# Optimization experiments

Measured on AMD Instinct MI355X. Metric: run time of the kernel, lower is better.

The kernel has to match this reference:

```python
import jax, jax.numpy as jnp
from jax import lax
import numpy as np

DN = ('NDHWC', 'DHWIO', 'NDHWC')

def conv3d(x, w, b, stride=1):
    return lax.conv_general_dilated(x, w, (stride,) * 3, 'SAME', dimension_numbers=DN) + b

def convT3d(x, w, b, stride=2):
    return lax.conv_transpose(x, w, (stride,) * 3, 'SAME', dimension_numbers=DN) + b

def prelu(x, a):
    return jnp.where(x > 0, x, a * x)

def bn(x, g, be, m, v):
    # keras BatchNormalization, inference mode, epsilon=1e-3
    return (x - m) * g * lax.rsqrt(v + 1e-3) + be

def res_unit(x, c1w, c1b, c2w, c2b, g, be, m, v, a):
    # VQVAEResidualUnit: relu(x + PReLU(BN(conv2(swish(conv1(x))))))
    h = jax.nn.swish(conv3d(x, c1w, c1b))
    h = prelu(bn(conv3d(h, c2w, c2b), g, be, m, v), a)
    return jax.nn.relu(x + h)

def _forward(x, ec0_w, ec0_b, er0_c1w, er0_c1b, er0_c2w, er0_c2b, er0_g, er0_be, er0_m, er0_v, er0_a, ec1_w, ec1_b, er1_c1w, er1_c1b, er1_c2w, er1_c2b, er1_g, er1_be, er1_m, er1_v, er1_a, eo_w, eo_b, eo_a, codebook, dc0_w, dc0_b, dc0_a, dr0_c1w, dr0_c1b, dr0_c2w, dr0_c2b, dr0_g, dr0_be, dr0_m, dr0_v, dr0_a, du0_w, du0_b, dr1_c1w, dr1_c1b, dr1_c2w, dr1_c2b, dr1_g, dr1_be, dr1_m, dr1_v, dr1_a, du1_w, du1_b):
    # ----- Encoder -----
    h = jax.nn.relu(conv3d(x, ec0_w, ec0_b, stride=2))   # [B,64,64,64,64]
    h = res_unit(h, er0_c1w, er0_c1b, er0_c2w, er0_c2b, er0_g, er0_be, er0_m, er0_v, er0_a)
    h = jax.nn.relu(conv3d(h, ec1_w, ec1_b, stride=2))   # [B,32,32,32,128]
    h = res_unit(h, er1_c1w, er1_c1b, er1_c2w, er1_c2b, er1_g, er1_be, er1_m, er1_v, er1_a)
    z = prelu(conv3d(h, eo_w, eo_b), eo_a)               # [B,32,32,32,64] latent
    # ----- NSVQ (inference: hard codebook lookup) -----
    D = z.shape[-1]
    flat = z.reshape(-1, D)                              # [N, 64], N = B*32^3
    dist = (flat * flat).sum(1, keepdims=True) + (codebook * codebook).sum(1) - 2.0 * (flat @ codebook.T)  # [N, K]
    idx = jnp.argmin(dist, axis=1)
    zq = codebook[idx].reshape(z.shape)
    K = codebook.shape[0]
    p = jnp.zeros((K,), jnp.float32).at[idx].add(1.0) / flat.shape[0]
    perplexity = jnp.exp(-jnp.sum(p * jnp.log(p + 1e-12)))
    # ----- Decoder -----
    h = prelu(conv3d(zq, dc0_w, dc0_b), dc0_a)           # [B,32,32,32,128]
    h = res_unit(h, dr0_c1w, dr0_c1b, dr0_c2w, dr0_c2b, dr0_g, dr0_be, dr0_m, dr0_v, dr0_a)
    h = jax.nn.relu(convT3d(h, du0_w, du0_b))            # [B,64,64,64,64]
    h = res_unit(h, dr1_c1w, dr1_c1b, dr1_c2w, dr1_c2b, dr1_g, dr1_be, dr1_m, dr1_v, dr1_a)
    recon = convT3d(h, du1_w, du1_b)                     # [B,128,128,128,1]
    return recon, perplexity

def setup_inputs() -> dict:
    key = jax.random.key(0)
    ks = iter(jax.random.split(key, 40))
    nrm = lambda *s: jax.random.normal(next(ks), s, jnp.float32) * 0.05
    def ru(pfx, c):
        return {pfx + '_c1w': nrm(3, 3, 3, c, c), pfx + '_c1b': jnp.zeros((c,), jnp.float32),
                pfx + '_c2w': nrm(3, 3, 3, c, c), pfx + '_c2b': jnp.zeros((c,), jnp.float32),
                pfx + '_g': jnp.ones((c,), jnp.float32), pfx + '_be': jnp.zeros((c,), jnp.float32),
                pfx + '_m': jnp.zeros((c,), jnp.float32), pfx + '_v': jnp.ones((c,), jnp.float32),
                pfx + '_a': jnp.full((c,), 0.25, jnp.float32)}
    C0, C1, D, K = 64, 128, 64, 512
    inp = {'x': jax.random.normal(next(ks), (2, 128, 128, 128, 1), jnp.float32)}
    inp.update(ec0_w=nrm(4, 4, 4, 1, C0), ec0_b=jnp.zeros((C0,), jnp.float32))
    inp.update(ru('er0', C0))
    inp.update(ec1_w=nrm(4, 4, 4, C0, C1), ec1_b=jnp.zeros((C1,), jnp.float32))
    inp.update(ru('er1', C1))
    inp.update(eo_w=nrm(3, 3, 3, C1, D), eo_b=jnp.zeros((D,), jnp.float32), eo_a=jnp.full((D,), 0.25, jnp.float32))
    inp.update(codebook=jax.random.uniform(next(ks), (K, D), jnp.float32, -1.0, 1.0) * np.sqrt(6.0 / D).astype(np.float32))
    inp.update(dc0_w=nrm(3, 3, 3, D, C1), dc0_b=jnp.zeros((C1,), jnp.float32), dc0_a=jnp.full((C1,), 0.25, jnp.float32))
    inp.update(ru('dr0', C1))
    inp.update(du0_w=nrm(4, 4, 4, C1, C0), du0_b=jnp.zeros((C0,), jnp.float32))
    inp.update(ru('dr1', C0))
    inp.update(du1_w=nrm(4, 4, 4, C0, 1), du1_b=jnp.zeros((1,), jnp.float32))
    return inp

def reference(x, ec0_w, ec0_b, er0_c1w, er0_c1b, er0_c2w, er0_c2b, er0_g, er0_be, er0_m, er0_v, er0_a, ec1_w, ec1_b, er1_c1w, er1_c1b, er1_c2w, er1_c2b, er1_g, er1_be, er1_m, er1_v, er1_a, eo_w, eo_b, eo_a, codebook, dc0_w, dc0_b, dc0_a, dr0_c1w, dr0_c1b, dr0_c2w, dr0_c2b, dr0_g, dr0_be, dr0_m, dr0_v, dr0_a, du0_w, du0_b, dr1_c1w, dr1_c1b, dr1_c2w, dr1_c2b, dr1_g, dr1_be, dr1_m, dr1_v, dr1_a, du1_w, du1_b):
    return _forward(x, ec0_w, ec0_b, er0_c1w, er0_c1b, er0_c2w, er0_c2b, er0_g, er0_be, er0_m, er0_v, er0_a, ec1_w, ec1_b, er1_c1w, er1_c1b, er1_c2w, er1_c2b, er1_g, er1_be, er1_m, er1_v, er1_a, eo_w, eo_b, eo_a, codebook, dc0_w, dc0_b, dc0_a, dr0_c1w, dr0_c1b, dr0_c2w, dr0_c2b, dr0_g, dr0_be, dr0_m, dr0_v, dr0_a, du0_w, du0_b, dr1_c1w, dr1_c1b, dr1_c2w, dr1_c2b, dr1_g, dr1_be, dr1_m, dr1_v, dr1_a, du1_w, du1_b)
```

## Files before the change

kernel.cpp:

```cpp
#include <hip/hip_runtime.h>
#include <cstdint>


typedef unsigned short bf16_t;
typedef __attribute__((ext_vector_type(8)))  short s8b;
typedef __attribute__((ext_vector_type(16))) float f32x16;

__device__ __forceinline__ float b2f(bf16_t u) { return __uint_as_float((unsigned)u << 16); }
__device__ __forceinline__ bf16_t f2b(float f) {
    unsigned x = __float_as_uint(f);
    return (bf16_t)((x + 0x7FFFu + ((x >> 16) & 1u)) >> 16);
}

__device__ __forceinline__ void split3s(float v, unsigned short& h,
                                        unsigned short& m, unsigned short& l)
{
    const unsigned uv = __float_as_uint(v);
    const float fh = __uint_as_float(uv & 0xFFFF0000u);
    const float r1 = v - fh;
    const unsigned u1 = __float_as_uint(r1);
    const float fm = __uint_as_float(u1 & 0xFFFF0000u);
    const float r2 = r1 - fm;
    h = (unsigned short)(uv >> 16);
    m = (unsigned short)(u1 >> 16);
    l = (unsigned short)(__float_as_uint(r2) >> 16);
}

__device__ __forceinline__ int wdst(int tap, int ci_, int co_, int ci, int co)
{
    const int ks = ci_ >> 4, half = (ci_ >> 3) & 1, j = ci_ & 7;
    return (((tap * (ci >> 4) + ks) * 2 + half) * co + co_) * 8 + j;
}

__global__ __launch_bounds__(256)
void wprep3(const float* __restrict__ w, bf16_t* __restrict__ h,
            bf16_t* __restrict__ m, bf16_t* __restrict__ l,
            int ci, int co, int n)
{
    const int i = blockIdx.x * 256 + threadIdx.x;
    if (i >= n) return;
    const int co_ = i % co;
    const int ci_ = (i / co) % ci;
    const int tap = i / (co * ci);
    const int dst = wdst(tap, ci_, co_, ci, co);
    unsigned short hh, mm, ll2;
    split3s(w[i], hh, mm, ll2);
    h[dst] = hh; m[dst] = mm; l[dst] = ll2;
}

__global__ __launch_bounds__(256)
void wprep_split(const float* __restrict__ w, bf16_t* __restrict__ hi,
                 bf16_t* __restrict__ lo, int ci, int co, int n)
{
    const int i = blockIdx.x * 256 + threadIdx.x;
    if (i >= n) return;
    const int co_ = i % co;
    const int ci_ = (i / co) % ci;
    const int tap = i / (co * ci);
    const float v = w[i];
    const int dst = wdst(tap, ci_, co_, ci, co);
    const bf16_t h = f2b(v);
    hi[dst] = h;
    lo[dst] = f2b(v - b2f(h));
}

template<int CIN, int COUT, int SD, int NW, int EPI>
__global__ __launch_bounds__((SD / 32) * NW * 64)
void conv3e(const float* __restrict__ xf,
            const bf16_t* __restrict__ wh, const bf16_t* __restrict__ wm,
            const bf16_t* __restrict__ wl,
            const float* __restrict__ bias,
            const float* __restrict__ g, const float* __restrict__ be,
            const float* __restrict__ mn, const float* __restrict__ vr,
            const float* __restrict__ al,
            const float* skf, float* __restrict__ of)
{
    constexpr int NT = (SD / 32) * NW * 64;
    constexpr int LP = (SD * CIN) / (4 * NT);
    constexpr int KS = CIN / 16;
    __shared__ bf16_t lh[SD * CIN], lm[SD * CIN], ll[SD * CIN];

    const int tid  = threadIdx.x;
    const int lane = tid & 63;
    const int wid  = tid >> 6;
    const int wn   = wid % NW, wm2 = wid / NW;
    const int half = lane >> 5, ln = lane & 31;
    const int w    = wm2 * 32 + ln;
    const int nwg  = gridDim.x;
    const int bid  = (blockIdx.x & 7) * (nwg >> 3) + (blockIdx.x >> 3);
    const int h    = bid % SD;
    const int d    = (bid / SD) % SD;
    const int b    = bid / (SD * SD);
    const int cout0 = wn * 64 + ln;

    int pz[9], py[9], pt[9], np = 0;
    for (int kd = 0; kd < 3; ++kd) {
        const int iz = d + kd - 1;
        if ((unsigned)iz >= (unsigned)SD) continue;
        for (int kh = 0; kh < 3; ++kh) {
            const int iy = h + kh - 1;
            if ((unsigned)iy >= (unsigned)SD) continue;
            pz[np] = iz; py[np] = iy; pt[np] = (kd * 3 + kh) * 3; ++np;
        }
    }

    f32x16 accA[2], accB[2];
#pragma unroll
    for (int i = 0; i < 16; ++i) {
        accA[0][i] = 0.f; accA[1][i] = 0.f;
        accB[0][i] = 0.f; accB[1][i] = 0.f;
    }

    float4 rg[LP];
    auto loadrow = [&](int iz, int iy) {
        const float* src = xf + ((size_t)((b * SD + iz) * SD + iy)) * SD * CIN;
#pragma unroll
        for (int j = 0; j < LP; ++j)
            rg[j] = *reinterpret_cast<const float4*>(src + (size_t)(tid + j * NT) * 4);
    };
    auto writerow = [&]() {
#pragma unroll
        for (int j = 0; j < LP; ++j) {
            const int idx = (tid + j * NT) * 4;
            const int vox = idx / CIN, ch = idx % CIN;
            ushort4 h4, m4, l4;
            split3s(rg[j].x, h4.x, m4.x, l4.x);
            split3s(rg[j].y, h4.y, m4.y, l4.y);
            split3s(rg[j].z, h4.z, m4.z, l4.z);
            split3s(rg[j].w, h4.w, m4.w, l4.w);
            const int bo = ((vox * CIN + ch) * 2) ^ ((vox & 7) << 4);
            *reinterpret_cast<ushort4*>((char*)&lh[0] + bo) = h4;
            *reinterpret_cast<ushort4*>((char*)&lm[0] + bo) = m4;
            *reinterpret_cast<ushort4*>((char*)&ll[0] + bo) = l4;
        }
    };

    loadrow(pz[0], py[0]);
    writerow();
    __syncthreads();
#pragma unroll 1
    for (int i = 0; i < np; ++i) {
        if (i + 1 < np) loadrow(pz[i + 1], py[i + 1]);
#pragma unroll
        for (int kw = 0; kw < 3; ++kw) {
            const int tap = pt[i] + kw;
            const int iw = w + kw - 1;
            const bool edge = (unsigned)iw >= (unsigned)SD;
            const int wcl = edge ? w : iw;
            const s8b zz = {};
#pragma unroll
            for (int ks = 0; ks < KS; ++ks) {
                const int bo = ((wcl * CIN + half * 8 + ks * 16) * 2) ^ ((wcl & 7) << 4);
                s8b ah  = *reinterpret_cast<const s8b*>((const char*)&lh[0] + bo);
                s8b am  = *reinterpret_cast<const s8b*>((const char*)&lm[0] + bo);
                s8b al3 = *reinterpret_cast<const s8b*>((const char*)&ll[0] + bo);
                if (edge) { ah = zz; am = zz; al3 = zz; }
                const size_t wb0 = ((size_t)((tap * KS + ks) * 2 + half) * COUT + cout0) * 8;
#pragma unroll
                for (int n2 = 0; n2 < 2; ++n2) {
                    const size_t wb = wb0 + n2 * 256;
                    const s8b bh = *reinterpret_cast<const s8b*>(wh + wb);
                    const s8b bm = *reinterpret_cast<const s8b*>(wm + wb);
                    const s8b bl = *reinterpret_cast<const s8b*>(wl + wb);
                    accA[n2] = __builtin_amdgcn_mfma_f32_32x32x16_bf16(ah, bh, accA[n2], 0, 0, 0);
                    accB[n2] = __builtin_amdgcn_mfma_f32_32x32x16_bf16(ah, bm, accB[n2], 0, 0, 0);
                    accA[n2] = __builtin_amdgcn_mfma_f32_32x32x16_bf16(am, bh, accA[n2], 0, 0, 0);
                    accB[n2] = __builtin_amdgcn_mfma_f32_32x32x16_bf16(am, bm, accB[n2], 0, 0, 0);
                    accA[n2] = __builtin_amdgcn_mfma_f32_32x32x16_bf16(al3, bh, accA[n2], 0, 0, 0);
                    accB[n2] = __builtin_amdgcn_mfma_f32_32x32x16_bf16(ah, bl, accB[n2], 0, 0, 0);
                }
            }
        }
        if (i + 1 < np) {
            __syncthreads();
            writerow();
            __syncthreads();
        }
    }

    const size_t outrow = ((size_t)((b * SD + d) * SD + h)) * SD;
#pragma unroll
    for (int n2 = 0; n2 < 2; ++n2) {
        const int cout = wn * 64 + n2 * 32 + ln;
        const float bv = bias[cout];
        float sc = 0.f, mm = 0.f, bb2 = 0.f, aa = 0.f;
        if constexpr (EPI == 3) {
            sc = g[cout] * (1.0f / sqrtf(vr[cout] + 1e-3f));
            mm = mn[cout]; bb2 = be[cout]; aa = al[cout];
        }
        if constexpr (EPI == 2) aa = al[cout];
#pragma unroll
        for (int r = 0; r < 16; ++r) {
            const int rl = (r & 3) + 8 * (r >> 2) + 4 * half;
            const size_t oe = (outrow + wm2 * 32 + rl) * COUT + cout;
            float y = accA[n2][r] + accB[n2][r] + bv;
            if constexpr (EPI == 0) y = fmaxf(y, 0.f);
            else if constexpr (EPI == 1) y = y / (1.f + expf(-y));
            else if constexpr (EPI == 2) y = y > 0.f ? y : aa * y;
            else {
                float t2 = (y - mm) * sc + bb2;
                t2 = t2 > 0.f ? t2 : aa * t2;
                y = fmaxf(skf[oe] + t2, 0.f);
            }
            of[oe] = y;
        }
    }
}

__global__ __launch_bounds__(128)
void convs2e(const float* __restrict__ xf,
             const bf16_t* __restrict__ wh, const bf16_t* __restrict__ wm,
             const bf16_t* __restrict__ wl,
             const float* __restrict__ bias, float* __restrict__ of)
{
    constexpr int NT = 128, LP = (64 * 64) / (4 * NT);
    __shared__ bf16_t lh[64 * 64], lm[64 * 64], ll[64 * 64];

    const int tid  = threadIdx.x;
    const int lane = tid & 63;
    const int wn   = tid >> 6;
    const int half = lane >> 5, ln = lane & 31;
    const int nwg  = gridDim.x;
    const int bid  = (blockIdx.x & 7) * (nwg >> 3) + (blockIdx.x >> 3);
    const int h    = bid % 32;
    const int d    = (bid / 32) % 32;
    const int b    = bid / 1024;
    const int cout0 = wn * 64 + ln;

    int pz[16], py[16], pt[16], np = 0;
    for (int kd = 0; kd < 4; ++kd) {
        const int iz = 2 * d + kd - 1;
        if ((unsigned)iz >= 64u) continue;
        for (int kh = 0; kh < 4; ++kh) {
            const int iy = 2 * h + kh - 1;
            if ((unsigned)iy >= 64u) continue;
            pz[np] = iz; py[np] = iy; pt[np] = (kd * 4 + kh) * 4; ++np;
        }
    }

    f32x16 accA[2], accB[2];
#pragma unroll
    for (int i = 0; i < 16; ++i) {
        accA[0][i] = 0.f; accA[1][i] = 0.f;
        accB[0][i] = 0.f; accB[1][i] = 0.f;
    }

    float4 rg[LP];
    auto loadrow = [&](int iz, int iy) {
        const float* src = xf + ((size_t)((b * 64 + iz) * 64 + iy)) * 64 * 64;
#pragma unroll
        for (int j = 0; j < LP; ++j)
            rg[j] = *reinterpret_cast<const float4*>(src + (size_t)(tid + j * NT) * 4);
    };
    auto writerow = [&]() {
#pragma unroll
        for (int j = 0; j < LP; ++j) {
            const int idx = (tid + j * NT) * 4;
            const int vox = idx / 64, ch = idx % 64;
            ushort4 h4, m4, l4;
            split3s(rg[j].x, h4.x, m4.x, l4.x);
            split3s(rg[j].y, h4.y, m4.y, l4.y);
            split3s(rg[j].z, h4.z, m4.z, l4.z);
            split3s(rg[j].w, h4.w, m4.w, l4.w);
            const int bo = ((vox * 64 + ch) * 2) ^ ((vox & 7) << 4);
            *reinterpret_cast<ushort4*>((char*)&lh[0] + bo) = h4;
            *reinterpret_cast<ushort4*>((char*)&lm[0] + bo) = m4;
            *reinterpret_cast<ushort4*>((char*)&ll[0] + bo) = l4;
        }
    };

    loadrow(pz[0], py[0]);
    writerow();
    __syncthreads();
#pragma unroll 1
    for (int i = 0; i < np; ++i) {
        if (i + 1 < np) loadrow(pz[i + 1], py[i + 1]);
#pragma unroll
        for (int kw = 0; kw < 4; ++kw) {
            const int tap = pt[i] + kw;
            const int iw = 2 * ln + kw - 1;
            const bool edge = (unsigned)iw >= 64u;
            const int wcl = edge ? 2 * ln : iw;
            const s8b zz = {};
#pragma unroll
            for (int ks = 0; ks < 4; ++ks) {
                const int bo = ((wcl * 64 + half * 8 + ks * 16) * 2) ^ ((wcl & 7) << 4);
                s8b ah  = *reinterpret_cast<const s8b*>((const char*)&lh[0] + bo);
                s8b am  = *reinterpret_cast<const s8b*>((const char*)&lm[0] + bo);
                s8b al3 = *reinterpret_cast<const s8b*>((const char*)&ll[0] + bo);
                if (edge) { ah = zz; am = zz; al3 = zz; }
                const size_t wb0 = ((size_t)((tap * 4 + ks) * 2 + half) * 128 + cout0) * 8;
#pragma unroll
                for (int n2 = 0; n2 < 2; ++n2) {
                    const size_t wb = wb0 + n2 * 256;
                    const s8b bh = *reinterpret_cast<const s8b*>(wh + wb);
                    const s8b bm = *reinterpret_cast<const s8b*>(wm + wb);
                    const s8b bl = *reinterpret_cast<const s8b*>(wl + wb);
                    accA[n2] = __builtin_amdgcn_mfma_f32_32x32x16_bf16(ah, bh, accA[n2], 0, 0, 0);
                    accB[n2] = __builtin_amdgcn_mfma_f32_32x32x16_bf16(ah, bm, accB[n2], 0, 0, 0);
                    accA[n2] = __builtin_amdgcn_mfma_f32_32x32x16_bf16(am, bh, accA[n2], 0, 0, 0);
                    accB[n2] = __builtin_amdgcn_mfma_f32_32x32x16_bf16(am, bm, accB[n2], 0, 0, 0);
                    accA[n2] = __builtin_amdgcn_mfma_f32_32x32x16_bf16(al3, bh, accA[n2], 0, 0, 0);
                    accB[n2] = __builtin_amdgcn_mfma_f32_32x32x16_bf16(ah, bl, accB[n2], 0, 0, 0);
                }
            }
        }
        if (i + 1 < np) {
            __syncthreads();
            writerow();
            __syncthreads();
        }
    }

    const size_t outrow = ((size_t)((b * 32 + d) * 32 + h)) * 32;
#pragma unroll
    for (int n2 = 0; n2 < 2; ++n2) {
        const int cout = wn * 64 + n2 * 32 + ln;
        const float bv = bias[cout];
#pragma unroll
        for (int r = 0; r < 16; ++r) {
            const int rl = (r & 3) + 8 * (r >> 2) + 4 * half;
            const size_t oe = (outrow + rl) * 128 + cout;
            of[oe] = fmaxf(accA[n2][r] + accB[n2][r] + bv, 0.f);
        }
    }
}

template<int CIN, int COUT, int SD, int NW, int EPI>
__global__ __launch_bounds__((SD / 32) * NW * 64)
void conv3d(const bf16_t* __restrict__ xh, const bf16_t* __restrict__ xl,
            const bf16_t* __restrict__ wh, const bf16_t* __restrict__ wl,
            const float* __restrict__ bias,
            const float* __restrict__ g, const float* __restrict__ be,
            const float* __restrict__ mn, const float* __restrict__ vr,
            const float* __restrict__ al,
            const bf16_t* skh, const bf16_t* skl,
            bf16_t* oh, bf16_t* ol)
{
    constexpr int NT = (SD / 32) * NW * 64;
    constexpr int LP = (SD * CIN) / (4 * NT);
    constexpr int KS = CIN / 16;
    __shared__ bf16_t lh[SD * CIN], ll[SD * CIN];

    const int tid  = threadIdx.x;
    const int lane = tid & 63;
    const int wid  = tid >> 6;
    const int wn   = wid % NW, wm2 = wid / NW;
    const int half = lane >> 5, ln = lane & 31;
    const int w    = wm2 * 32 + ln;
    const int nwg  = gridDim.x;
    const int bid  = (blockIdx.x & 7) * (nwg >> 3) + (blockIdx.x >> 3);
    const int h    = bid % SD;
    const int d    = (bid / SD) % SD;
    const int b    = bid / (SD * SD);
    const int cout0 = wn * 64 + ln;

    int pz[9], py[9], pt[9], np = 0;
    for (int kd = 0; kd < 3; ++kd) {
        const int iz = d + kd - 1;
        if ((unsigned)iz >= (unsigned)SD) continue;
        for (int kh = 0; kh < 3; ++kh) {
            const int iy = h + kh - 1;
            if ((unsigned)iy >= (unsigned)SD) continue;
            pz[np] = iz; py[np] = iy; pt[np] = (kd * 3 + kh) * 3; ++np;
        }
    }

    f32x16 accA[2], accB[2];
#pragma unroll
    for (int i = 0; i < 16; ++i) {
        accA[0][i] = 0.f; accA[1][i] = 0.f;
        accB[0][i] = 0.f; accB[1][i] = 0.f;
    }

    ushort4 rh[LP], rl2[LP];
    auto loadrow = [&](int iz, int iy) {
        const size_t rb = ((size_t)((b * SD + iz) * SD + iy)) * SD * CIN;
#pragma unroll
        for (int j = 0; j < LP; ++j) {
            const int idx = (tid + j * NT) * 4;
            rh[j]  = *reinterpret_cast<const ushort4*>(xh + rb + idx);
            rl2[j] = *reinterpret_cast<const ushort4*>(xl + rb + idx);
        }
    };
    auto writerow = [&]() {
#pragma unroll
        for (int j = 0; j < LP; ++j) {
            const int idx = (tid + j * NT) * 4;
            const int vox = idx / CIN, ch = idx % CIN;
            const int bo = ((vox * CIN + ch) * 2) ^ ((vox & 7) << 4);
            *reinterpret_cast<ushort4*>((char*)&lh[0] + bo) = rh[j];
            *reinterpret_cast<ushort4*>((char*)&ll[0] + bo) = rl2[j];
        }
    };

    loadrow(pz[0], py[0]);
    writerow();
    __syncthreads();
#pragma unroll 1
    for (int i = 0; i < np; ++i) {
        if (i + 1 < np) loadrow(pz[i + 1], py[i + 1]);
#pragma unroll
        for (int kw = 0; kw < 3; ++kw) {
            const int tap = pt[i] + kw;
            const int iw = w + kw - 1;
            const bool edge = (unsigned)iw >= (unsigned)SD;
            const int wcl = edge ? w : iw;
            const s8b zz = {};
#pragma unroll
            for (int ks = 0; ks < KS; ++ks) {
                const int bo = ((wcl * CIN + half * 8 + ks * 16) * 2) ^ ((wcl & 7) << 4);
                s8b ah  = *reinterpret_cast<const s8b*>((const char*)&lh[0] + bo);
                s8b al2 = *reinterpret_cast<const s8b*>((const char*)&ll[0] + bo);
                if (edge) { ah = zz; al2 = zz; }
                const size_t wb0 = ((size_t)((tap * KS + ks) * 2 + half) * COUT + cout0) * 8;
#pragma unroll
                for (int n2 = 0; n2 < 2; ++n2) {
                    const size_t wb = wb0 + n2 * 256;
                    const s8b bh = *reinterpret_cast<const s8b*>(wh + wb);
                    const s8b bl = *reinterpret_cast<const s8b*>(wl + wb);
                    accA[n2] = __builtin_amdgcn_mfma_f32_32x32x16_bf16(ah, bh, accA[n2], 0, 0, 0);
                    accB[n2] = __builtin_amdgcn_mfma_f32_32x32x16_bf16(al2, bh, accB[n2], 0, 0, 0);
                    accB[n2] = __builtin_amdgcn_mfma_f32_32x32x16_bf16(ah, bl, accB[n2], 0, 0, 0);
                }
            }
        }
        if (i + 1 < np) {
            __syncthreads();
            writerow();
            __syncthreads();
        }
    }

    const size_t outrow = ((size_t)((b * SD + d) * SD + h)) * SD;
#pragma unroll
    for (int n2 = 0; n2 < 2; ++n2) {
        const int cout = wn * 64 + n2 * 32 + ln;
        const float bv = bias[cout];
        float sc = 0.f, mm = 0.f, bb2 = 0.f, aa = 0.f;
        if constexpr (EPI == 3) {
            sc = g[cout] * (1.0f / sqrtf(vr[cout] + 1e-3f));
            mm = mn[cout]; bb2 = be[cout]; aa = al[cout];
        }
        if constexpr (EPI == 2) aa = al[cout];
#pragma unroll
        for (int r = 0; r < 16; ++r) {
            const int rl = (r & 3) + 8 * (r >> 2) + 4 * half;
            const size_t oe = (outrow + wm2 * 32 + rl) * COUT + cout;
            float y = accA[n2][r] + accB[n2][r] + bv;
            if constexpr (EPI == 0) y = fmaxf(y, 0.f);
            else if constexpr (EPI == 1) y = y / (1.f + expf(-y));
            else if constexpr (EPI == 2) y = y > 0.f ? y : aa * y;
            else {
                float t2 = (y - mm) * sc + bb2;
                t2 = t2 > 0.f ? t2 : aa * t2;
                float sv = b2f(skh[oe]) + b2f(skl[oe]);
                y = fmaxf(sv + t2, 0.f);
            }
            const bf16_t hh = f2b(y);
            oh[oe] = hh;
            ol[oe] = f2b(y - b2f(hh));
        }
    }
}

__global__ __launch_bounds__(256)
void convTm(const bf16_t* __restrict__ xh, const bf16_t* __restrict__ xl,
            const bf16_t* __restrict__ wh, const bf16_t* __restrict__ wl,
            const float* __restrict__ bias,
            bf16_t* __restrict__ oh, bf16_t* __restrict__ ol)
{
    constexpr int NT = 256, LP = (32 * 128) / (4 * NT);
    __shared__ bf16_t lh[32 * 128], ll[32 * 128];

    const int tid  = threadIdx.x;
    const int lane = tid & 63;
    const int wid  = tid >> 6;
    const int wn   = wid & 1, p = wid >> 1;
    const int half = lane >> 5, ln = lane & 31;
    const int nwg  = gridDim.x;
    const int bid  = (blockIdx.x & 7) * (nwg >> 3) + (blockIdx.x >> 3);
    const int ohh  = bid % 64;
    const int od   = (bid / 64) % 64;
    const int b    = bid / 4096;
    const int pd = od & 1, dz = od >> 1;
    const int ph = ohh & 1, hy = ohh >> 1;
    const int cout = wn * 32 + ln;

    int pz[4], py[4], pt[4], np = 0;
    for (int jd = 0; jd < 2; ++jd) {
        const int kd = pd + 2 * jd;
        const int iz = dz + pd - 1 + jd;
        if ((unsigned)iz >= 32u) continue;
        for (int jh = 0; jh < 2; ++jh) {
            const int kh = ph + 2 * jh;
            const int iy = hy + ph - 1 + jh;
            if ((unsigned)iy >= 32u) continue;
            pz[np] = iz; py[np] = iy; pt[np] = (kd * 4 + kh) * 4; ++np;
        }
    }

    f32x16 accA, accB;
#pragma unroll
    for (int i = 0; i < 16; ++i) { accA[i] = 0.0f; accB[i] = 0.0f; }

    ushort4 rh[LP], rl2[LP];
    auto loadrow = [&](int iz, int iy) {
        const size_t rb = ((size_t)((b * 32 + iz) * 32 + iy)) * 32 * 128;
#pragma unroll
        for (int j = 0; j < LP; ++j) {
            const int idx = (tid + j * NT) * 4;
            rh[j]  = *reinterpret_cast<const ushort4*>(xh + rb + idx);
            rl2[j] = *reinterpret_cast<const ushort4*>(xl + rb + idx);
        }
    };
    auto writerow = [&]() {
#pragma unroll
        for (int j = 0; j < LP; ++j) {
            const int idx = (tid + j * NT) * 4;
            const int vox = idx / 128, ch = idx % 128;
            const int bo = ((vox * 128 + ch) * 2) ^ ((vox & 7) << 4);
            *reinterpret_cast<ushort4*>((char*)&lh[0] + bo) = rh[j];
            *reinterpret_cast<ushort4*>((char*)&ll[0] + bo) = rl2[j];
        }
    };

    loadrow(pz[0], py[0]);
    writerow();
    __syncthreads();
#pragma unroll 1
    for (int i = 0; i < np; ++i) {
        if (i + 1 < np) loadrow(pz[i + 1], py[i + 1]);
#pragma unroll
        for (int jw = 0; jw < 2; ++jw) {
            const int kw = p + 2 * jw;
            const int tap = pt[i] + kw;
            const int ix = ln + p - 1 + jw;
            const bool edge = (unsigned)ix >= 32u;
            const int xcl = edge ? ln : ix;
            const s8b zz = {};
#pragma unroll
            for (int ks = 0; ks < 8; ++ks) {
                const int bo = ((xcl * 128 + half * 8 + ks * 16) * 2) ^ ((xcl & 7) << 4);
                s8b a  = *reinterpret_cast<const s8b*>((const char*)&lh[0] + bo);
                s8b a2 = *reinterpret_cast<const s8b*>((const char*)&ll[0] + bo);
                if (edge) { a = zz; a2 = zz; }
                const size_t wb = ((size_t)((tap * 8 + ks) * 2 + half) * 64 + cout) * 8;
                const s8b bb = *reinterpret_cast<const s8b*>(wh + wb);
                const s8b b2 = *reinterpret_cast<const s8b*>(wl + wb);
                accA = __builtin_amdgcn_mfma_f32_32x32x16_bf16(a, bb, accA, 0, 0, 0);
                accB = __builtin_amdgcn_mfma_f32_32x32x16_bf16(a2, bb, accB, 0, 0, 0);
                accB = __builtin_amdgcn_mfma_f32_32x32x16_bf16(a, b2, accB, 0, 0, 0);
            }
        }
        if (i + 1 < np) {
            __syncthreads();
            writerow();
            __syncthreads();
        }
    }

    const float bv = bias[cout];
#pragma unroll
    for (int r = 0; r < 16; ++r) {
        const int rl = (r & 3) + 8 * (r >> 2) + 4 * half;
        const int ow = 2 * rl + p;
        const size_t oe = (((size_t)((b * 64 + od) * 64 + ohh)) * 64 + ow) * 64 + cout;
        const float y = fmaxf(accA[r] + accB[r] + bv, 0.f);
        const bf16_t hh = f2b(y);
        oh[oe] = hh;
        ol[oe] = f2b(y - b2f(hh));
    }
}

__global__ __launch_bounds__(256)
void conv_ec0f(const float* __restrict__ in, const float* __restrict__ wt,
               const float* __restrict__ bias, float* __restrict__ out)
{
    const int co  = threadIdx.x;
    const int vox = blockIdx.x * 4 + threadIdx.y;
    const int w = vox % 64; int rem = vox / 64;
    const int h = rem % 64; rem /= 64;
    const int d = rem % 64; rem /= 64;
    const int b = rem;
    float acc[4] = {0.f, 0.f, 0.f, 0.f};
#pragma unroll 1
    for (int kd = 0; kd < 4; ++kd) {
        const int iz = 2 * d + kd - 1;
        if ((unsigned)iz >= 128u) continue;
#pragma unroll 1
        for (int kh = 0; kh < 4; ++kh) {
            const int iy = 2 * h + kh - 1;
            if ((unsigned)iy >= 128u) continue;
#pragma unroll
            for (int kw = 0; kw < 4; ++kw) {
                const int ix = 2 * w + kw - 1;
                if ((unsigned)ix >= 128u) continue;
                const float xv = in[(size_t)((b * 128 + iz) * 128 + iy) * 128 + ix];
                acc[kw] = fmaf(xv, wt[((kd * 4 + kh) * 4 + kw) * 64 + co], acc[kw]);
            }
        }
    }
    const float s = (acc[0] + acc[1]) + (acc[2] + acc[3]) + bias[co];
    out[(size_t)vox * 64 + co] = fmaxf(s, 0.f);
}

__global__ __launch_bounds__(256)
void convT_du1w(const bf16_t* __restrict__ inh, const bf16_t* __restrict__ inl,
                const float* __restrict__ wt, const float* __restrict__ bias,
                float* __restrict__ out)
{
    const int lane = threadIdx.x & 63;
    const int wv   = blockIdx.x * 4 + (threadIdx.x >> 6);
    const size_t obase = (size_t)wv * 16;
    const int ow0 = (int)(obase % 128);
    size_t rem = obase / 128;
    const int ohh = (int)(rem % 128); rem /= 128;
    const int od  = (int)(rem % 128); rem /= 128;
    const int b   = (int)rem;
    const int pd = od & 1, dz = od >> 1;
    const int ph = ohh & 1, hy = ohh >> 1;
    const int wx0 = ow0 >> 1;

    float acc[16];
#pragma unroll
    for (int o = 0; o < 16; ++o) acc[o] = 0.f;

#pragma unroll
    for (int jd = 0; jd < 2; ++jd) {
        const int kd = pd + 2 * jd;
        const int iz = dz + pd - 1 + jd;
        if ((unsigned)iz >= 64u) continue;
#pragma unroll
        for (int jh = 0; jh < 2; ++jh) {
            const int kh = ph + 2 * jh;
            const int iy = hy + ph - 1 + jh;
            if ((unsigned)iy >= 64u) continue;
            const size_t rbase = ((size_t)((b * 64 + iz) * 64 + iy)) * 64;
            float wv4[4];
#pragma unroll
            for (int kw = 0; kw < 4; ++kw)
                wv4[kw] = wt[(size_t)((kd * 4 + kh) * 4 + kw) * 64 + lane];
            float v[10];
#pragma unroll
            for (int t = 0; t < 10; ++t) {
                const int ix = wx0 - 1 + t;
                if ((unsigned)ix < 64u) {
                    const size_t a = (rbase + ix) * 64 + lane;
                    v[t] = b2f(inh[a]) + b2f(inl[a]);
                } else {
                    v[t] = 0.f;
                }
            }
#pragma unroll
            for (int o = 0; o < 16; ++o) {
                const int pw = o & 1;
                const int t0 = (o >> 1) + pw;
                acc[o] = fmaf(v[t0],     wv4[pw],     acc[o]);
                acc[o] = fmaf(v[t0 + 1], wv4[pw + 2], acc[o]);
            }
        }
    }

    const float b0 = bias[0];
#pragma unroll
    for (int o = 0; o < 16; ++o) {
        float s = acc[o];
        s += __shfl_xor(s, 1);
        s += __shfl_xor(s, 2);
        s += __shfl_xor(s, 4);
        s += __shfl_xor(s, 8);
        s += __shfl_xor(s, 16);
        s += __shfl_xor(s, 32);
        if (lane == 0) out[obase + o] = s + b0;
    }
}

__global__ void zero512(float* __restrict__ p) { p[threadIdx.x] = 0.0f; }

__global__ void vq_cnorm(const float* __restrict__ cb, float* __restrict__ cnorm)
{
    const int k = blockIdx.x * 64 + threadIdx.x;
    float s = 0.0f;
    for (int ci = 0; ci < 64; ++ci) { const float c = cb[k * 64 + ci]; s = fmaf(c, c, s); }
    cnorm[k] = s;
}

__global__ __launch_bounds__(256)
void vq_assign(const float* __restrict__ z, const float* __restrict__ cb,
               const float* __restrict__ cnorm, int* __restrict__ idx,
               float* __restrict__ hist, int N)
{
    const int n = blockIdx.x * 256 + threadIdx.x;
    const float4* zp = reinterpret_cast<const float4*>(z + (size_t)n * 64);
    float4 zv[16];
    float z2 = 0.0f;
#pragma unroll
    for (int i = 0; i < 16; ++i) {
        zv[i] = zp[i];
        z2 += zv[i].x * zv[i].x + zv[i].y * zv[i].y + zv[i].z * zv[i].z + zv[i].w * zv[i].w;
    }
    float best = 3.4e38f;
    int bi = 0;
#pragma unroll 1
    for (int k = 0; k < 512; ++k) {
        const float4* cp = reinterpret_cast<const float4*>(cb + (size_t)k * 64);
        float dot = 0.0f;
#pragma unroll
        for (int i = 0; i < 16; ++i) {
            const float4 c = cp[i];
            dot += zv[i].x * c.x + zv[i].y * c.y + zv[i].z * c.z + zv[i].w * c.w;
        }
        const float dist = z2 + cnorm[k] - 2.0f * dot;
        if (dist < best) { best = dist; bi = k; }
    }
    idx[n] = bi;
    atomicAdd(&hist[bi], 1.0f);
}

__global__ __launch_bounds__(256)
void vq_gather_split(const float* __restrict__ cb, const int* __restrict__ idx,
                     bf16_t* __restrict__ zh, bf16_t* __restrict__ zl)
{
    const int gid = blockIdx.x * 256 + threadIdx.x;
    const int n = gid >> 4, c4 = gid & 15;
    const int k = idx[n];
    const float4 c = reinterpret_cast<const float4*>(cb)[k * 16 + c4];
    ushort4 h, l;
    h.x = f2b(c.x); l.x = f2b(c.x - b2f(h.x));
    h.y = f2b(c.y); l.y = f2b(c.y - b2f(h.y));
    h.z = f2b(c.z); l.z = f2b(c.z - b2f(h.z));
    h.w = f2b(c.w); l.w = f2b(c.w - b2f(h.w));
    reinterpret_cast<ushort4*>(zh)[gid] = h;
    reinterpret_cast<ushort4*>(zl)[gid] = l;
}

__global__ __launch_bounds__(512)
void perplexity_k(const float* __restrict__ hist, float* __restrict__ out, float invN)
{
    __shared__ float red[512];
    const int t = threadIdx.x;
    const float p = hist[t] * invN;
    red[t] = p * logf(p + 1e-12f);
    __syncthreads();
    for (int s = 256; s > 0; s >>= 1) {
        if (t < s) red[t] += red[t + s];
        __syncthreads();
    }
    if (t == 0) out[0] = expf(-red[0]);
}

extern "C" void kernel_launch(void* const* d_in, const int* in_sizes, int n_in,
                              void* d_out, int out_size, void* d_ws, size_t ws_size,
                              hipStream_t stream)
{
    const float* x       = (const float*)d_in[0];
    const float* ec0_w   = (const float*)d_in[1];
    const float* ec0_b   = (const float*)d_in[2];
    const float* er0_c1w = (const float*)d_in[3];
    const float* er0_c1b = (const float*)d_in[4];
    const float* er0_c2w = (const float*)d_in[5];
    const float* er0_c2b = (const float*)d_in[6];
    const float* er0_g   = (const float*)d_in[7];
    const float* er0_be  = (const float*)d_in[8];
    const float* er0_m   = (const float*)d_in[9];
    const float* er0_v   = (const float*)d_in[10];
    const float* er0_a   = (const float*)d_in[11];
    const float* ec1_w   = (const float*)d_in[12];
    const float* ec1_b   = (const float*)d_in[13];
    const float* er1_c1w = (const float*)d_in[14];
    const float* er1_c1b = (const float*)d_in[15];
    const float* er1_c2w = (const float*)d_in[16];
    const float* er1_c2b = (const float*)d_in[17];
    const float* er1_g   = (const float*)d_in[18];
    const float* er1_be  = (const float*)d_in[19];
    const float* er1_m   = (const float*)d_in[20];
    const float* er1_v   = (const float*)d_in[21];
    const float* er1_a   = (const float*)d_in[22];
    const float* eo_w    = (const float*)d_in[23];
    const float* eo_b    = (const float*)d_in[24];
    const float* eo_a    = (const float*)d_in[25];
    const float* cb      = (const float*)d_in[26];
    const float* dc0_w   = (const float*)d_in[27];
    const float* dc0_b   = (const float*)d_in[28];
    const float* dc0_a   = (const float*)d_in[29];
    const float* dr0_c1w = (const float*)d_in[30];
    const float* dr0_c1b = (const float*)d_in[31];
    const float* dr0_c2w = (const float*)d_in[32];
    const float* dr0_c2b = (const float*)d_in[33];
    const float* dr0_g   = (const float*)d_in[34];
    const float* dr0_be  = (const float*)d_in[35];
    const float* dr0_m   = (const float*)d_in[36];
    const float* dr0_v   = (const float*)d_in[37];
    const float* dr0_a   = (const float*)d_in[38];
    const float* du0_w   = (const float*)d_in[39];
    const float* du0_b   = (const float*)d_in[40];
    const float* dr1_c1w = (const float*)d_in[41];
    const float* dr1_c1b = (const float*)d_in[42];
    const float* dr1_c2w = (const float*)d_in[43];
    const float* dr1_c2b = (const float*)d_in[44];
    const float* dr1_g   = (const float*)d_in[45];
    const float* dr1_be  = (const float*)d_in[46];
    const float* dr1_m   = (const float*)d_in[47];
    const float* dr1_v   = (const float*)d_in[48];
    const float* dr1_a   = (const float*)d_in[49];
    const float* du1_w   = (const float*)d_in[50];
    const float* du1_b   = (const float*)d_in[51];

    float* out = (float*)d_out;

    char* W = (char*)d_ws;
    float*  Af  = (float*)(W);
    float*  Hf  = (float*)(W + 134217728);
    float*  E1f = (float*)(W + 134217728);
    float*  R1f = (float*)(W + 134217728 + 33554432);
    float*  Zf  = (float*)(W);
    int*    IDX = (int*)  (W + 16777216);
    float*  CN  = (float*)(W + 17039360);
    float*  HS  = (float*)(W + 17041408);
    bf16_t* ZQh = (bf16_t*)(W + 33554432);
    bf16_t* ZQl = (bf16_t*)(W + 41943040);
    bf16_t* D0h = (bf16_t*)(W + 50331648);
    bf16_t* D0l = (bf16_t*)(W + 67108864);
    bf16_t* Gh  = (bf16_t*)(W + 83886080);
    bf16_t* Gl  = (bf16_t*)(W + 100663296);
    bf16_t* U0h = (bf16_t*)(W + 134217728);
    bf16_t* U0l = (bf16_t*)(W + 201326592);
    bf16_t* G1h = (bf16_t*)(W);
    bf16_t* G1l = (bf16_t*)(W + 67108864);

    char* WB = (char*)d_out;
    bf16_t* e0c1h = (bf16_t*)(WB + 0);
    bf16_t* e0c1m = (bf16_t*)(WB + 221184);
    bf16_t* e0c1l = (bf16_t*)(WB + 442368);
    bf16_t* e0c2h = (bf16_t*)(WB + 663552);
    bf16_t* e0c2m = (bf16_t*)(WB + 884736);
    bf16_t* e0c2l = (bf16_t*)(WB + 1105920);
    bf16_t* ec1h  = (bf16_t*)(WB + 1327104);
    bf16_t* ec1m  = (bf16_t*)(WB + 2375680);
    bf16_t* ec1l  = (bf16_t*)(WB + 3424256);
    bf16_t* e1c1h = (bf16_t*)(WB + 4472832);
    bf16_t* e1c1m = (bf16_t*)(WB + 5357568);
    bf16_t* e1c1l = (bf16_t*)(WB + 6242304);
    bf16_t* e1c2h = (bf16_t*)(WB + 7127040);
    bf16_t* e1c2m = (bf16_t*)(WB + 8011776);
    bf16_t* e1c2l = (bf16_t*)(WB + 8896512);
    bf16_t* eoh   = (bf16_t*)(WB + 9781248);
    bf16_t* eom   = (bf16_t*)(WB + 10223616);
    bf16_t* eol   = (bf16_t*)(WB + 10665984);
    bf16_t* dc0h  = (bf16_t*)(WB + 0);
    bf16_t* dc0l  = (bf16_t*)(WB + 442368);
    bf16_t* d0c1h = (bf16_t*)(WB + 884736);
    bf16_t* d0c1l = (bf16_t*)(WB + 1769472);
    bf16_t* d0c2h = (bf16_t*)(WB + 2654208);
    bf16_t* d0c2l = (bf16_t*)(WB + 3538944);
    bf16_t* du0h  = (bf16_t*)(WB + 4423680);
    bf16_t* du0l  = (bf16_t*)(WB + 5472256);
    bf16_t* d1c1h = (bf16_t*)(WB + 6520832);
    bf16_t* d1c1l = (bf16_t*)(WB + 6742016);
    bf16_t* d1c2h = (bf16_t*)(WB + 6963200);
    bf16_t* d1c2l = (bf16_t*)(WB + 7184384);

    const float* fn = nullptr;
    const bf16_t* bn_ = nullptr;

    wprep3<<<432, 256, 0, stream>>>(er0_c1w, e0c1h, e0c1m, e0c1l, 64, 64, 110592);
    wprep3<<<432, 256, 0, stream>>>(er0_c2w, e0c2h, e0c2m, e0c2l, 64, 64, 110592);
    wprep3<<<2048, 256, 0, stream>>>(ec1_w, ec1h, ec1m, ec1l, 64, 128, 524288);
    wprep3<<<1728, 256, 0, stream>>>(er1_c1w, e1c1h, e1c1m, e1c1l, 128, 128, 442368);
    wprep3<<<1728, 256, 0, stream>>>(er1_c2w, e1c2h, e1c2m, e1c2l, 128, 128, 442368);
    wprep3<<<864, 256, 0, stream>>>(eo_w, eoh, eom, eol, 128, 64, 221184);

    conv_ec0f<<<131072, dim3(64, 4), 0, stream>>>(x, ec0_w, ec0_b, Af);

    conv3e<64, 64, 64, 1, 1><<<8192, 128, 0, stream>>>(
        Af, e0c1h, e0c1m, e0c1l, er0_c1b, fn, fn, fn, fn, fn, fn, Hf);
    conv3e<64, 64, 64, 1, 3><<<8192, 128, 0, stream>>>(
        Hf, e0c2h, e0c2m, e0c2l, er0_c2b, er0_g, er0_be, er0_m, er0_v, er0_a, Af, Af);

    convs2e<<<2048, 128, 0, stream>>>(Af, ec1h, ec1m, ec1l, ec1_b, E1f);

    conv3e<128, 128, 32, 2, 1><<<2048, 128, 0, stream>>>(
        E1f, e1c1h, e1c1m, e1c1l, er1_c1b, fn, fn, fn, fn, fn, fn, R1f);
    conv3e<128, 128, 32, 2, 3><<<2048, 128, 0, stream>>>(
        R1f, e1c2h, e1c2m, e1c2l, er1_c2b, er1_g, er1_be, er1_m, er1_v, er1_a, E1f, E1f);

    conv3e<128, 64, 32, 1, 2><<<2048, 64, 0, stream>>>(
        E1f, eoh, eom, eol, eo_b, fn, fn, fn, fn, eo_a, fn, Zf);

    vq_cnorm<<<8, 64, 0, stream>>>(cb, CN);
    zero512<<<1, 512, 0, stream>>>(HS);
    vq_assign<<<256, 256, 0, stream>>>(Zf, cb, CN, IDX, HS, 65536);
    perplexity_k<<<1, 512, 0, stream>>>(HS, out + 4194304, 1.0f / 65536.0f);
    vq_gather_split<<<4096, 256, 0, stream>>>(cb, IDX, ZQh, ZQl);

    wprep_split<<<864, 256, 0, stream>>>(dc0_w, dc0h, dc0l, 64, 128, 221184);
    wprep_split<<<1728, 256, 0, stream>>>(dr0_c1w, d0c1h, d0c1l, 128, 128, 442368);
    wprep_split<<<1728, 256, 0, stream>>>(dr0_c2w, d0c2h, d0c2l, 128, 128, 442368);
    wprep_split<<<2048, 256, 0, stream>>>(du0_w, du0h, du0l, 128, 64, 524288);
    wprep_split<<<432, 256, 0, stream>>>(dr1_c1w, d1c1h, d1c1l, 64, 64, 110592);
    wprep_split<<<432, 256, 0, stream>>>(dr1_c2w, d1c2h, d1c2l, 64, 64, 110592);

    conv3d<64, 128, 32, 2, 2><<<2048, 128, 0, stream>>>(
        ZQh, ZQl, dc0h, dc0l, dc0_b, fn, fn, fn, fn, dc0_a, bn_, bn_, D0h, D0l);
    conv3d<128, 128, 32, 2, 1><<<2048, 128, 0, stream>>>(
        D0h, D0l, d0c1h, d0c1l, dr0_c1b, fn, fn, fn, fn, fn, bn_, bn_, Gh, Gl);
    conv3d<128, 128, 32, 2, 3><<<2048, 128, 0, stream>>>(
        Gh, Gl, d0c2h, d0c2l, dr0_c2b, dr0_g, dr0_be, dr0_m, dr0_v, dr0_a,
        D0h, D0l, D0h, D0l);

    convTm<<<8192, 256, 0, stream>>>(D0h, D0l, du0h, du0l, du0_b, U0h, U0l);

    conv3d<64, 64, 64, 1, 1><<<8192, 128, 0, stream>>>(
        U0h, U0l, d1c1h, d1c1l, dr1_c1b, fn, fn, fn, fn, fn, bn_, bn_, G1h, G1l);
    conv3d<64, 64, 64, 1, 3><<<8192, 128, 0, stream>>>(
        G1h, G1l, d1c2h, d1c2l, dr1_c2b, dr1_g, dr1_be, dr1_m, dr1_v, dr1_a,
        U0h, U0l, U0h, U0l);

    convT_du1w<<<65536, 256, 0, stream>>>(U0h, U0l, du1_w, du1_b, out);
}
```

Before: 6.203 ms.

## Rewrite first strided conv as bf16x3 MFMA GEMM with LDS-staged input rows

```diff
diff --git a/kernel.cpp b/kernel.cpp
--- a/kernel.cpp
+++ b/kernel.cpp
@@ -573,36 +573,96 @@
     }
 }
 
-__global__ __launch_bounds__(256)
-void conv_ec0f(const float* __restrict__ in, const float* __restrict__ wt,
-               const float* __restrict__ bias, float* __restrict__ out)
-{
-    const int co  = threadIdx.x;
-    const int vox = blockIdx.x * 4 + threadIdx.y;
-    const int w = vox % 64; int rem = vox / 64;
-    const int h = rem % 64; rem /= 64;
-    const int d = rem % 64; rem /= 64;
-    const int b = rem;
-    float acc[4] = {0.f, 0.f, 0.f, 0.f};
-#pragma unroll 1
-    for (int kd = 0; kd < 4; ++kd) {
-        const int iz = 2 * d + kd - 1;
-        if ((unsigned)iz >= 128u) continue;
-#pragma unroll 1
-        for (int kh = 0; kh < 4; ++kh) {
-            const int iy = 2 * h + kh - 1;
-            if ((unsigned)iy >= 128u) continue;
-#pragma unroll
-            for (int kw = 0; kw < 4; ++kw) {
-                const int ix = 2 * w + kw - 1;
-                if ((unsigned)ix >= 128u) continue;
-                const float xv = in[(size_t)((b * 128 + iz) * 128 + iy) * 128 + ix];
-                acc[kw] = fmaf(xv, wt[((kd * 4 + kh) * 4 + kw) * 64 + co], acc[kw]);
-            }
-        }
-    }
-    const float s = (acc[0] + acc[1]) + (acc[2] + acc[3]) + bias[co];
-    out[(size_t)vox * 64 + co] = fmaxf(s, 0.f);
+__global__ __launch_bounds__(128)
+void conv_ec0m(const float* __restrict__ x,
+               const bf16_t* __restrict__ wh, const bf16_t* __restrict__ wm,
+               const bf16_t* __restrict__ wl,
+               const float* __restrict__ bias, float* __restrict__ of)
+{
+    __shared__ bf16_t lh[16 * 132], lm[16 * 132], ll[16 * 132];
+
+    const int tid  = threadIdx.x;
+    const int lane = tid & 63;
+    const int wm2  = tid >> 6;
+    const int half = lane >> 5, ln = lane & 31;
+    const int w    = wm2 * 32 + ln;
+    const int nwg  = gridDim.x;
+    const int bid  = (blockIdx.x & 7) * (nwg >> 3) + (blockIdx.x >> 3);
+    const int h    = bid % 64;
+    const int d    = (bid / 64) % 64;
+    const int b    = bid / 4096;
+
+    for (int i = tid; i < 16 * 132; i += 128) {
+        const int row = i / 132, col = i % 132;
+        const int kd = row >> 2, kh = row & 3;
+        const int iz = 2 * d + kd - 1, iy = 2 * h + kh - 1;
+        const int ix = col - 1;
+        float v = 0.f;
+        if ((unsigned)iz < 128u && (unsigned)iy < 128u &&
+            (unsigned)ix < 128u && col < 130)
+            v = x[(size_t)((b * 128 + iz) * 128 + iy) * 128 + ix];
+        unsigned short hh, mm2, ll2;
+        split3s(v, hh, mm2, ll2);
+        lh[i] = hh; lm[i] = mm2; ll[i] = ll2;
+    }
+    __syncthreads();
+
+    f32x16 accA[2], accB[2];
+#pragma unroll
+    for (int i = 0; i < 16; ++i) {
+        accA[0][i] = 0.f; accA[1][i] = 0.f;
+        accB[0][i] = 0.f; accB[1][i] = 0.f;
+    }
+
+#pragma unroll
+    for (int ks = 0; ks < 4; ++ks) {
+        const int row0 = ks * 4 + 2 * half;
+        const int i0 = row0 * 132 + 2 * w;
+        const int i1 = i0 + 132;
+        s8b ah, am, al3;
+        {
+            uint* ap = (uint*)&ah;
+            ap[0] = *(const uint*)&lh[i0]; ap[1] = *(const uint*)&lh[i0 + 2];
+            ap[2] = *(const uint*)&lh[i1]; ap[3] = *(const uint*)&lh[i1 + 2];
+        }
+        {
+            uint* ap = (uint*)&am;
+            ap[0] = *(const uint*)&lm[i0]; ap[1] = *(const uint*)&lm[i0 + 2];
+            ap[2] = *(const uint*)&lm[i1]; ap[3] = *(const uint*)&lm[i1 + 2];
+        }
+        {
+            uint* ap = (uint*)&al3;
+            ap[0] = *(const uint*)&ll[i0]; ap[1] = *(const uint*)&ll[i0 + 2];
+            ap[2] = *(const uint*)&ll[i1]; ap[3] = *(const uint*)&ll[i1 + 2];
+        }
+        const size_t wb0 = ((size_t)(ks * 2 + half) * 64 + ln) * 8;
+#pragma unroll
+        for (int n2 = 0; n2 < 2; ++n2) {
+            const size_t wb = wb0 + n2 * 256;
+            const s8b bh = *reinterpret_cast<const s8b*>(wh + wb);
+            const s8b bm = *reinterpret_cast<const s8b*>(wm + wb);
+            const s8b bl = *reinterpret_cast<const s8b*>(wl + wb);
+            accA[n2] = __builtin_amdgcn_mfma_f32_32x32x16_bf16(ah, bh, accA[n2], 0, 0, 0);
+            accB[n2] = __builtin_amdgcn_mfma_f32_32x32x16_bf16(ah, bm, accB[n2], 0, 0, 0);
+            accA[n2] = __builtin_amdgcn_mfma_f32_32x32x16_bf16(am, bh, accA[n2], 0, 0, 0);
+            accB[n2] = __builtin_amdgcn_mfma_f32_32x32x16_bf16(am, bm, accB[n2], 0, 0, 0);
+            accA[n2] = __builtin_amdgcn_mfma_f32_32x32x16_bf16(al3, bh, accA[n2], 0, 0, 0);
+            accB[n2] = __builtin_amdgcn_mfma_f32_32x32x16_bf16(ah, bl, accB[n2], 0, 0, 0);
+        }
+    }
+
+    const size_t outrow = ((size_t)((b * 64 + d) * 64 + h)) * 64;
+#pragma unroll
+    for (int n2 = 0; n2 < 2; ++n2) {
+        const int cout = n2 * 32 + ln;
+        const float bv = bias[cout];
+#pragma unroll
+        for (int r = 0; r < 16; ++r) {
+            const int rl = (r & 3) + 8 * (r >> 2) + 4 * half;
+            const size_t oe = (outrow + wm2 * 32 + rl) * 64 + cout;
+            of[oe] = fmaxf(accA[n2][r] + accB[n2][r] + bv, 0.f);
+        }
+    }
 }
 
 __global__ __launch_bounds__(256)
@@ -848,6 +908,9 @@
     bf16_t* eoh   = (bf16_t*)(WB + 9781248);
     bf16_t* eom   = (bf16_t*)(WB + 10223616);
     bf16_t* eol   = (bf16_t*)(WB + 10665984);
+    bf16_t* wec0h = (bf16_t*)(WB + 11108352);
+    bf16_t* wec0m = (bf16_t*)(WB + 11116544);
+    bf16_t* wec0l = (bf16_t*)(WB + 11124736);
     bf16_t* dc0h  = (bf16_t*)(WB + 0);
     bf16_t* dc0l  = (bf16_t*)(WB + 442368);
     bf16_t* d0c1h = (bf16_t*)(WB + 884736);
@@ -864,6 +927,7 @@
     const float* fn = nullptr;
     const bf16_t* bn_ = nullptr;
 
+    wprep3<<<16, 256, 0, stream>>>(ec0_w, wec0h, wec0m, wec0l, 64, 64, 4096);
     wprep3<<<432, 256, 0, stream>>>(er0_c1w, e0c1h, e0c1m, e0c1l, 64, 64, 110592);
     wprep3<<<432, 256, 0, stream>>>(er0_c2w, e0c2h, e0c2m, e0c2l, 64, 64, 110592);
     wprep3<<<2048, 256, 0, stream>>>(ec1_w, ec1h, ec1m, ec1l, 64, 128, 524288);
@@ -871,7 +935,7 @@
     wprep3<<<1728, 256, 0, stream>>>(er1_c2w, e1c2h, e1c2m, e1c2l, 128, 128, 442368);
     wprep3<<<864, 256, 0, stream>>>(eo_w, eoh, eom, eol, 128, 64, 221184);
 
-    conv_ec0f<<<131072, dim3(64, 4), 0, stream>>>(x, ec0_w, ec0_b, Af);
+    conv_ec0m<<<8192, 128, 0, stream>>>(x, wec0h, wec0m, wec0l, ec0_b, Af);
 
     conv3e<64, 64, 64, 1, 1><<<8192, 128, 0, stream>>>(
         Af, e0c1h, e0c1m, e0c1l, er0_c1b, fn, fn, fn, fn, fn, fn, Hf);
```

Result: faster. 5.506 ms (-11.2%).
